# Kernel tuning notes

Measured on AMD Instinct MI355X. Metric: run time of the kernel, lower is better.

## Reference

```python
import jax, jax.numpy as jnp
import numpy as np

NUM_HEADS = 8
TOPK = 16


def setup_inputs() -> dict:
    key = jax.random.key(0)
    ks = jax.random.split(key, 13)
    B, C, H, W = 2, 512, 64, 64
    Hu, Wu = H // 2, W // 2
    hd = C // NUM_HEADS
    n = lambda k, shape, s=1.0: jax.random.normal(k, shape, dtype=jnp.float32) * s
    return {
        "x": n(ks[0], (B, C, H, W)),
        "upper_feat": n(ks[1], (B, C, Hu, Wu)),
        "gumbel": jax.random.gumbel(ks[2], (B, NUM_HEADS, Hu * Wu), dtype=jnp.float32),
        # 1x1 convs (Conv2d + folded eval-mode BN => weight matrix + bias)
        "q_w": n(ks[3], (C, C), 0.02), "q_b": n(ks[4], (C,), 0.02),
        "kv_w": n(ks[5], (2 * C, C), 0.02), "kv_b": n(ks[6], (2 * C,), 0.02),
        "proj_w": n(ks[7], (C, C), 0.02), "proj_b": n(ks[8], (C,), 0.02),
        # depthwise 7x7 PE conv (groups = C)
        "pe_w": n(ks[9], (C, 1, 7, 7), 0.02), "pe_b": n(ks[10], (C,), 0.02),
        # gate conv1d kernel_size=1: [head_dim, 2*head_dim]
        "gate_w": n(ks[11], (hd, 2 * hd), 0.02), "gate_b": n(ks[12], (hd,), 0.02),
    }


def reference(x, upper_feat, gumbel, q_w, q_b, kv_w, kv_b, proj_w, proj_b,
              pe_w, pe_b, gate_w, gate_b):
    B, C, H, W = x.shape
    hd = C // NUM_HEADS
    Hu, Wu = upper_feat.shape[2], upper_feat.shape[3]
    N, Nu = H * W, Hu * Wu
    scale = hd ** -0.5

    def conv1x1(t, w, b):
        return jnp.einsum('bchw,oc->bohw', t, w) + b[None, :, None, None]

    # coarse attention: q from x, k/v from upper_feat
    q = conv1x1(x, q_w, q_b).reshape(B, NUM_HEADS, hd, N).transpose(0, 1, 3, 2)          # [B,h,N,d]
    kv = conv1x1(upper_feat, kv_w, kv_b).reshape(B, NUM_HEADS, 2 * hd, Nu).transpose(0, 1, 3, 2)
    k, v = kv[..., :hd], kv[..., hd:]                                                    # [B,h,Nu,d]
    sim = jnp.einsum('bhnd,bhmd->bhnm', q, k) * scale                                    # [B,h,N,Nu]
    attn = jax.nn.softmax(sim, axis=-1)
    coarse = jnp.einsum('bhnm,bhmd->bhnd', attn, v)                                      # [B,h,N,d]

    # fine branch: kv from x, top-k token selection via gumbel-softmax scores
    f_kv = conv1x1(x, kv_w, kv_b).reshape(B, NUM_HEADS, 2 * hd, N).transpose(0, 1, 3, 2)
    f_k, f_v = f_kv[..., :hd], f_kv[..., hd:]                                            # [B,h,N,d]

    # heat: channel-mean of x, adaptive-avg-pooled 2x2 to upper resolution (no grad)
    heat = jax.lax.stop_gradient(
        x.mean(axis=1).reshape(B, Hu, 2, Wu, 2).mean(axis=(2, 4)).reshape(B, Nu))
    global_sim = sim.mean(axis=2) * heat[:, None, :]                                     # [B,h,Nu]
    soft_weights = jax.nn.softmax(global_sim + gumbel, axis=-1)
    _, idx = jax.lax.top_k(soft_weights, TOPK)                                           # [B,h,K]

    # map each selected upper-token to its 2x2 block of x-tokens
    h_idx = (idx // Wu) * 2
    w_idx = (idx % Wu) * 2
    idx_full = jnp.concatenate(
        [(h_idx + dh) * W + (w_idx + dw) for dh in range(2) for dw in range(2)], axis=-1)  # [B,h,4K]

    topk_k = jnp.take_along_axis(f_k, idx_full[..., None], axis=2)                       # [B,h,4K,d]
    topk_v = jnp.take_along_axis(f_v, idx_full[..., None], axis=2)
    fine = jax.nn.softmax(jnp.einsum('bhnd,bhmd->bhnm', q, topk_k) * scale, axis=-1)
    refined = jnp.einsum('bhnm,bhmd->bhnd', fine, topk_v)                                # [B,h,N,d]

    # gated fusion (conv1d kernel_size=1 == per-token linear over 2d channels)
    fusion = jnp.concatenate([coarse, refined], axis=-1)                                 # [B,h,N,2d]
    gate = jax.nn.sigmoid(jnp.einsum('bhnc,oc->bhno', fusion, gate_w) + gate_b)
    out = gate * refined + (1.0 - gate) * coarse                                         # [B,h,N,d]

    x_out = out.transpose(0, 1, 3, 2).reshape(B, C, H, W)

    # positional encoding: depthwise 7x7 conv on v, bilinear upsample to (H,W)
    v_rs = v.transpose(0, 1, 3, 2).reshape(B, C, Hu, Wu)
    v_pe = jax.lax.conv_general_dilated(
        v_rs, pe_w, (1, 1), ((3, 3), (3, 3)), feature_group_count=C,
        dimension_numbers=('NCHW', 'OIHW', 'NCHW')) + pe_b[None, :, None, None]
    v_pe = jax.image.resize(v_pe, (B, C, H, W), method='bilinear')

    return conv1x1(x_out + v_pe, proj_w, proj_b)
```

## Files before the change

### kernel.cpp

```cpp
#include <hip/hip_runtime.h>
#include <hip/hip_bf16.h>
#include <cstdint>

typedef __hip_bfloat16 bf16;
typedef unsigned short u16;
typedef __attribute__((ext_vector_type(8))) short bf16x8;
typedef __attribute__((ext_vector_type(4))) float f32x4;

static __device__ __forceinline__ float bs2f(u16 s) {
  unsigned int u = ((unsigned int)s) << 16;
  float f;
  __builtin_memcpy(&f, &u, 4);
  return f;
}
static __device__ __forceinline__ u16 f2bs(float f) {
  bf16 h = __float2bfloat16(f);
  u16 s;
  __builtin_memcpy(&s, &h, 2);
  return s;
}
static __device__ __forceinline__ float ldf(const void* p, size_t i, int f32) {
  return f32 ? ((const float*)p)[i] : bs2f(((const u16*)p)[i]);
}

__global__ __launch_bounds__(256) void detect_dtype(const uint4* __restrict__ xs,
                                                    int* __restrict__ flag) {
  int i = blockIdx.x * 256 + threadIdx.x;
  uint4 v = xs[i];
  bool hit = false;
#pragma unroll
  for (int j = 0; j < 4; ++j) {
    unsigned w = (j == 0) ? v.x : (j == 1) ? v.y : (j == 2) ? v.z : v.w;
    if ((w & 0x7F80u) == 0x7F80u) hit = true;
    if ((w & 0x7F800000u) == 0x7F800000u) hit = true;
  }
  unsigned long long mask = __ballot(hit);
  if (mask != 0ull && (threadIdx.x & 63) == 0) atomicOr(flag, 1);
}

__global__ __launch_bounds__(256) void prep_gate(
    const void* __restrict__ gate_w, const void* __restrict__ gate_b,
    u16* __restrict__ gwb, float* __restrict__ gbf,
    const int* __restrict__ dtf) {
  const int f32 = *dtf;
  int t = threadIdx.x;
  for (int i = t; i < 8192; i += 256)
    gwb[i] = f32 ? f2bs(((const float*)gate_w)[i]) : ((const u16*)gate_w)[i];
  if (t < 64) gbf[t] = ldf(gate_b, t, f32);
}

__global__ __launch_bounds__(256) void transpose_bf16(
    const void* __restrict__ src, u16* __restrict__ dst, int N,
    float* __restrict__ heat, const int* __restrict__ dtf) {
  const int f32 = *dtf;
  const int b = blockIdx.z, n0 = blockIdx.x * 64, c0 = blockIdx.y * 64;
  const int t = threadIdx.x;
  __shared__ __align__(16) u16 tile[64][72];
#pragma unroll
  for (int j = 0; j < 2; ++j) {
    int cc = (t >> 3) + j * 32;
    int nn = (t & 7) * 8;
    u16 tmp[8];
    if (f32) {
      const float* s4 = (const float*)src + ((size_t)(b * 512 + c0 + cc)) * N + n0 + nn;
#pragma unroll
      for (int u = 0; u < 8; ++u) tmp[u] = f2bs(s4[u]);
    } else {
      *reinterpret_cast<uint4*>(tmp) = *reinterpret_cast<const uint4*>(
          (const u16*)src + ((size_t)(b * 512 + c0 + cc)) * N + n0 + nn);
    }
    *reinterpret_cast<uint4*>(&tile[cc][nn]) = *reinterpret_cast<const uint4*>(tmp);
  }
  __syncthreads();
  if (heat != nullptr && t < 32) {
    float s = 0.f;
#pragma unroll 8
    for (int cc = 0; cc < 64; ++cc)
      s += bs2f(tile[cc][2 * t]) + bs2f(tile[cc][2 * t + 1]);
    int y = blockIdx.x;
    atomicAdd(&heat[b * 1024 + (y >> 1) * 32 + t], s);
  }
#pragma unroll
  for (int j = 0; j < 2; ++j) {
    int nn = (t >> 3) + j * 32;
    int cc0 = (t & 7) * 8;
    u16 tmp[8];
#pragma unroll
    for (int u = 0; u < 8; ++u) tmp[u] = tile[cc0 + u][nn];
    *reinterpret_cast<uint4*>(&dst[((size_t)b * N + n0 + nn) * 512 + c0 + cc0]) =
        *reinterpret_cast<const uint4*>(tmp);
  }
}

template<int MODE>
__global__ __launch_bounds__(256) void gemm128(
    const u16* __restrict__ A, const void* __restrict__ W,
    const void* __restrict__ bias, u16* __restrict__ o0,
    void* __restrict__ ob, float* __restrict__ qsum, int M,
    const int* __restrict__ dtf) {
  const int f32 = *dtf;
  const int b = blockIdx.z, m0 = blockIdx.x * 128, oo0 = blockIdx.y * 64;
  const int t = threadIdx.x, w = t >> 6, lane = t & 63;
  const int quad = lane >> 4, c = lane & 15;
  __shared__ __align__(16) u16 As[128][72];
  __shared__ __align__(16) u16 Ws[64][72];
  f32x4 acc[2][4];
#pragma unroll
  for (int nt = 0; nt < 2; ++nt)
#pragma unroll
    for (int ot = 0; ot < 4; ++ot) acc[nt][ot] = (f32x4){0.f, 0.f, 0.f, 0.f};
  const u16* Ab = A + (size_t)b * M * 512;
  const int arow = t >> 1, acol = (t & 1) * 32;
  const int wrow = t >> 2, wcol = (t & 3) * 16;

  for (int k0 = 0; k0 < 512; k0 += 64) {
    __syncthreads();
    {
      const u16* ga = Ab + (size_t)(m0 + arow) * 512 + k0 + acol;
      uint4* ad = reinterpret_cast<uint4*>(&As[arow][acol]);
      const uint4* gs = reinterpret_cast<const uint4*>(ga);
      ad[0] = gs[0]; ad[1] = gs[1]; ad[2] = gs[2]; ad[3] = gs[3];
      if (f32) {
        const float* gw = (const float*)W + (size_t)(oo0 + wrow) * 512 + k0 + wcol;
#pragma unroll
        for (int e = 0; e < 16; ++e) Ws[wrow][wcol + e] = f2bs(gw[e]);
      } else {
        const u16* gw = (const u16*)W + (size_t)(oo0 + wrow) * 512 + k0 + wcol;
        *reinterpret_cast<uint4*>(&Ws[wrow][wcol])     = *reinterpret_cast<const uint4*>(gw);
        *reinterpret_cast<uint4*>(&Ws[wrow][wcol + 8]) = *reinterpret_cast<const uint4*>(gw + 8);
      }
    }
    __syncthreads();
#pragma unroll
    for (int ks = 0; ks < 2; ++ks) {
      bf16x8 av[2];
      av[0] = *reinterpret_cast<const bf16x8*>(&As[w * 32 + c][ks * 32 + quad * 8]);
      av[1] = *reinterpret_cast<const bf16x8*>(&As[w * 32 + 16 + c][ks * 32 + quad * 8]);
#pragma unroll
      for (int ot = 0; ot < 4; ++ot) {
        bf16x8 wv = *reinterpret_cast<const bf16x8*>(&Ws[ot * 16 + c][ks * 32 + quad * 8]);
#pragma unroll
        for (int nt = 0; nt < 2; ++nt) {
          if (MODE == 3)
            acc[nt][ot] = __builtin_amdgcn_mfma_f32_16x16x32_bf16(wv, av[nt], acc[nt][ot], 0, 0, 0);
          else
            acc[nt][ot] = __builtin_amdgcn_mfma_f32_16x16x32_bf16(av[nt], wv, acc[nt][ot], 0, 0, 0);
        }
      }
    }
  }

  if (MODE == 0) {
    const int h = oo0 >> 6, bh = b * 8 + h;
#pragma unroll
    for (int ot = 0; ot < 4; ++ot) {
      int o = oo0 + ot * 16 + c;
      int d = o & 63;
      float bv = ldf(bias, o, f32);
      float qs = 0.f;
#pragma unroll
      for (int nt = 0; nt < 2; ++nt)
#pragma unroll
        for (int r = 0; r < 4; ++r) {
          int m = m0 + w * 32 + nt * 16 + quad * 4 + r;
          float qv = acc[nt][ot][r] + bv;
          o0[((size_t)bh * M + m) * 64 + d] = f2bs(qv * 0.125f);
          qs += qv;
        }
      qs += __shfl_xor(qs, 16, 64);
      qs += __shfl_xor(qs, 32, 64);
      if (quad == 0) atomicAdd(&qsum[bh * 64 + d], qs);
    }
  } else {
#pragma unroll
    for (int ot = 0; ot < 4; ++ot)
#pragma unroll
      for (int r = 0; r < 4; ++r) {
        int o = oo0 + ot * 16 + quad * 4 + r;
        float bv = ldf(bias, o, f32);
#pragma unroll
        for (int nt = 0; nt < 2; ++nt) {
          int m = m0 + w * 32 + nt * 16 + c;
          float val = acc[nt][ot][r] + bv;
          size_t oi_ = ((size_t)(b * 512 + o)) * M + m;
          if (f32) ((float*)ob)[oi_] = val;
          else     ((u16*)ob)[oi_] = f2bs(val);
        }
      }
  }
}

__global__ __launch_bounds__(256) void gemm_kv(
    const u16* __restrict__ A, const void* __restrict__ W,
    const void* __restrict__ bias, u16* __restrict__ kb, u16* __restrict__ v2,
    int M, const int* __restrict__ dtf) {
  const int f32 = *dtf;
  const int b = blockIdx.z, m0 = blockIdx.x * 64, oo0 = blockIdx.y * 64;
  const int t = threadIdx.x, w = t >> 6, lane = t & 63;
  const int quad = lane >> 4, c = lane & 15;
  __shared__ __align__(16) u16 As[64][72];
  __shared__ __align__(16) u16 Ws[64][72];
  f32x4 acc[4];
#pragma unroll
  for (int ot = 0; ot < 4; ++ot) acc[ot] = (f32x4){0.f, 0.f, 0.f, 0.f};
  const u16* Ab = A + (size_t)b * M * 512;
  const int srow = t >> 2, scol = (t & 3) * 16;

  for (int k0 = 0; k0 < 512; k0 += 64) {
    __syncthreads();
    {
      const u16* ga = Ab + (size_t)(m0 + srow) * 512 + k0 + scol;
      *reinterpret_cast<uint4*>(&As[srow][scol])     = *reinterpret_cast<const uint4*>(ga);
      *reinterpret_cast<uint4*>(&As[srow][scol + 8]) = *reinterpret_cast<const uint4*>(ga + 8);
      if (f32) {
        const float* gw = (const float*)W + (size_t)(oo0 + srow) * 512 + k0 + scol;
#pragma unroll
        for (int e = 0; e < 16; ++e) Ws[srow][scol + e] = f2bs(gw[e]);
      } else {
        const u16* gw = (const u16*)W + (size_t)(oo0 + srow) * 512 + k0 + scol;
        *reinterpret_cast<uint4*>(&Ws[srow][scol])     = *reinterpret_cast<const uint4*>(gw);
        *reinterpret_cast<uint4*>(&Ws[srow][scol + 8]) = *reinterpret_cast<const uint4*>(gw + 8);
      }
    }
    __syncthreads();
#pragma unroll
    for (int ks = 0; ks < 2; ++ks) {
      bf16x8 av = *reinterpret_cast<const bf16x8*>(&As[w * 16 + c][ks * 32 + quad * 8]);
#pragma unroll
      for (int ot = 0; ot < 4; ++ot) {
        bf16x8 wv = *reinterpret_cast<const bf16x8*>(&Ws[ot * 16 + c][ks * 32 + quad * 8]);
        acc[ot] = __builtin_amdgcn_mfma_f32_16x16x32_bf16(av, wv, acc[ot], 0, 0, 0);
      }
    }
  }

#pragma unroll
  for (int ot = 0; ot < 4; ++ot) {
    int o = oo0 + ot * 16 + c;
    float bv = ldf(bias, o, f32);
    int hh = o >> 7, jj = o & 127;
#pragma unroll
    for (int r = 0; r < 4; ++r) {
      int m = m0 + w * 16 + quad * 4 + r;
      u16 val = f2bs(acc[ot][r] + bv);
      if (jj < 64) {
        kb[((size_t)(b * 8 + hh) * M + m) * 64 + jj] = val;
      } else {
        int d = jj & 63;
        v2[((((size_t)(b * 8 + hh) * 16 + (m >> 6)) * 2 + ((m >> 5) & 1)) * 4 + (d >> 4)) * 512
           + (((m >> 3) & 3) * 16 + (d & 15)) * 8 + (m & 7)] = val;
      }
    }
  }
}

__global__ __launch_bounds__(256) void topk_kernel(
    const float* __restrict__ qsum, const u16* __restrict__ k,
    const float* __restrict__ heat, const void* __restrict__ gumbel,
    int* __restrict__ posb, const int* __restrict__ dtf) {
  const int f32 = *dtf;
  int bh = blockIdx.x, b = bh >> 3, t = threadIdx.x;
  __shared__ float qs[64];
  __shared__ float s[1024];
  __shared__ float rv[256];
  __shared__ int   ri[256];
  if (t < 64) qs[t] = qsum[bh * 64 + t];
  __syncthreads();
  for (int j = 0; j < 4; ++j) {
    int m = t + j * 256;
    const u16* kr = k + ((size_t)bh * 1024 + m) * 64;
    float dot = 0.f;
    for (int d = 0; d < 64; ++d) dot += qs[d] * bs2f(kr[d]);
    s[m] = dot * (0.125f / 4096.0f) * (heat[b * 1024 + m] * (1.0f / 2048.0f)) +
           ldf(gumbel, (size_t)bh * 1024 + m, f32);
  }
  __syncthreads();
  for (int it = 0; it < 16; ++it) {
    float bv = -1e30f; int bi = 0x7fffffff;
    for (int j = 0; j < 4; ++j) {
      int m = t + j * 256; float vv = s[m];
      if (vv > bv || (vv == bv && m < bi)) { bv = vv; bi = m; }
    }
    rv[t] = bv; ri[t] = bi; __syncthreads();
    for (int off = 128; off; off >>= 1) {
      if (t < off) {
        if (rv[t + off] > rv[t] || (rv[t + off] == rv[t] && ri[t + off] < ri[t])) {
          rv[t] = rv[t + off]; ri[t] = ri[t + off];
        }
      }
      __syncthreads();
    }
    if (t == 0) {
      int mi = ri[0]; s[mi] = -1e30f;
      int hy = (mi >> 5) * 2, wx = (mi & 31) * 2;
      posb[bh * 64 + it]      = hy * 64 + wx;
      posb[bh * 64 + 16 + it] = hy * 64 + wx + 1;
      posb[bh * 64 + 32 + it] = (hy + 1) * 64 + wx;
      posb[bh * 64 + 48 + it] = (hy + 1) * 64 + wx + 1;
    }
    __syncthreads();
  }
}

__global__ __launch_bounds__(256) void gather_kv_mfma(
    const u16* __restrict__ xT, const void* __restrict__ kv_w,
    const void* __restrict__ kv_b, const int* __restrict__ posb,
    u16* __restrict__ tkb, u16* __restrict__ tvTb,
    const int* __restrict__ dtf) {
  const int f32 = *dtf;
  const int bh = blockIdx.x, b = bh >> 3, h = bh & 7;
  const int half = blockIdx.y;
  const int t = threadIdx.x, w = t >> 6, lane = t & 63;
  const int quad = lane >> 4, c = lane & 15;
  __shared__ int pos[64];
  __shared__ __align__(16) u16 As[64][72];
  __shared__ __align__(16) u16 Ws[64][72];
  if (t < 64) pos[t] = posb[bh * 64 + t];
  __syncthreads();
  const int obase = h * 128 + half * 64;
  const int srow = t >> 2, scol = (t & 3) * 16;
  const int arow = pos[srow];
  f32x4 acc[4];
#pragma unroll
  for (int ot = 0; ot < 4; ++ot) acc[ot] = (f32x4){0.f, 0.f, 0.f, 0.f};

  for (int k0 = 0; k0 < 512; k0 += 64) {
    __syncthreads();
    {
      const u16* ga = xT + ((size_t)b * 4096 + arow) * 512 + k0 + scol;
      *reinterpret_cast<uint4*>(&As[srow][scol])     = *reinterpret_cast<const uint4*>(ga);
      *reinterpret_cast<uint4*>(&As[srow][scol + 8]) = *reinterpret_cast<const uint4*>(ga + 8);
      if (f32) {
        const float* gw = (const float*)kv_w + (size_t)(obase + srow) * 512 + k0 + scol;
#pragma unroll
        for (int e = 0; e < 16; ++e) Ws[srow][scol + e] = f2bs(gw[e]);
      } else {
        const u16* gw = (const u16*)kv_w + (size_t)(obase + srow) * 512 + k0 + scol;
        *reinterpret_cast<uint4*>(&Ws[srow][scol])     = *reinterpret_cast<const uint4*>(gw);
        *reinterpret_cast<uint4*>(&Ws[srow][scol + 8]) = *reinterpret_cast<const uint4*>(gw + 8);
      }
    }
    __syncthreads();
#pragma unroll
    for (int ks = 0; ks < 2; ++ks) {
      bf16x8 av = *reinterpret_cast<const bf16x8*>(&As[w * 16 + c][ks * 32 + quad * 8]);
#pragma unroll
      for (int ot = 0; ot < 4; ++ot) {
        bf16x8 wv = *reinterpret_cast<const bf16x8*>(&Ws[ot * 16 + c][ks * 32 + quad * 8]);
        acc[ot] = __builtin_amdgcn_mfma_f32_16x16x32_bf16(av, wv, acc[ot], 0, 0, 0);
      }
    }
  }

#pragma unroll
  for (int ot = 0; ot < 4; ++ot) {
    int d = ot * 16 + c;
    float bv = ldf(kv_b, obase + d, f32);
#pragma unroll
    for (int r = 0; r < 4; ++r) {
      int m = w * 16 + quad * 4 + r;
      u16 val = f2bs(acc[ot][r] + bv);
      if (half) tvTb[((size_t)bh * 64 + d) * 64 + m] = val;
      else      tkb[((size_t)bh * 64 + m) * 64 + d] = val;
    }
  }
}

__global__ __launch_bounds__(256) void dwconv_kernel(
    const u16* __restrict__ v2, const void* __restrict__ pe_w,
    const void* __restrict__ pe_b, u16* __restrict__ vpe,
    const int* __restrict__ dtf) {
  const int f32 = *dtf;
  int bc = blockIdx.x;
  int b = bc >> 9, c = bc & 511;
  int h = c >> 6, d = c & 63;
  int dt = d >> 4, cc = d & 15;
  int t = threadIdx.x;
  __shared__ float img[1024];
  __shared__ float wts[49];
  if (t < 128) {
    int ch = t >> 3, s = (t >> 2) & 1, q2 = t & 3;
    const u16* src = v2 + ((((size_t)(b * 8 + h) * 16 + ch) * 2 + s) * 4 + dt) * 512
                        + (q2 * 16 + cc) * 8;
    uint4 v4 = *reinterpret_cast<const uint4*>(src);
    u16 tmp[8];
    *reinterpret_cast<uint4*>(tmp) = v4;
#pragma unroll
    for (int e = 0; e < 8; ++e) img[t * 8 + e] = bs2f(tmp[e]);
  }
  if (t < 49) wts[t] = ldf(pe_w, c * 49 + t, f32);
  float bias = ldf(pe_b, c, f32);
  __syncthreads();
  for (int i = t; i < 1024; i += 256) {
    int y = i >> 5, xx = i & 31;
    float a = 0.f;
#pragma unroll
    for (int ky = 0; ky < 7; ++ky) {
      int yy = y + ky - 3;
      if ((unsigned)yy >= 32u) continue;
#pragma unroll
      for (int kx = 0; kx < 7; ++kx) {
        int xc = xx + kx - 3;
        if ((unsigned)xc >= 32u) continue;
        a += img[yy * 32 + xc] * wts[ky * 7 + kx];
      }
    }
    vpe[(size_t)bc * 1024 + i] = f2bs(a + bias);
  }
}

__global__ __launch_bounds__(256, 4) void attn_fused(
    const u16* __restrict__ q, const u16* __restrict__ k,
    const u16* __restrict__ v2, const u16* __restrict__ tkb,
    const u16* __restrict__ tvTb, const u16* __restrict__ gwb,
    const float* __restrict__ gbf, const u16* __restrict__ vpe,
    u16* __restrict__ xsT) {
  const int bh = blockIdx.y, b = bh >> 3, h = bh & 7;
  const int bx = blockIdx.x;
  const int n0 = bx * 64;
  const int t = threadIdx.x, w = t >> 6, lane = t & 63;
  const int quad = lane >> 4, c = lane & 15;

  __shared__ __align__(16) u16 lds[13824];
  u16* Ks = lds;
  u16* Ps = lds + 9216;

  bf16x8 bq[2];
  {
    const u16* qr = q + ((size_t)bh * 4096 + n0 + w * 16 + c) * 64;
    bq[0] = *reinterpret_cast<const bf16x8*>(qr + quad * 8);
    bq[1] = *reinterpret_cast<const bf16x8*>(qr + 32 + quad * 8);
  }
  f32x4 po[4];
#pragma unroll
  for (int dt = 0; dt < 4; ++dt) po[dt] = (f32x4){0.f, 0.f, 0.f, 0.f};
  float sume = 0.f;

  const u16* kbase = k + (size_t)bh * 65536;
  const u16* v2base = v2 + (size_t)bh * 65536;
  const int srow = t >> 2, scol = (t & 3) * 16;

  uint4 kr0, kr1;
  {
    const u16* gk = kbase + (size_t)srow * 64 + scol;
    kr0 = *reinterpret_cast<const uint4*>(gk);
    kr1 = *reinterpret_cast<const uint4*>(gk + 8);
    *reinterpret_cast<uint4*>(&Ks[srow * 72 + scol])     = kr0;
    *reinterpret_cast<uint4*>(&Ks[srow * 72 + scol + 8]) = kr1;
    const u16* gk1 = kbase + (size_t)(64 + srow) * 64 + scol;
    kr0 = *reinterpret_cast<const uint4*>(gk1);
    kr1 = *reinterpret_cast<const uint4*>(gk1 + 8);
  }

  for (int ch = 0; ch < 16; ++ch) {
    __syncthreads();
    const int buf = ch & 1;

    bf16x8 av[4][2];
    {
      const u16* v2c = v2base + (size_t)ch * 4096;
#pragma unroll
      for (int dt = 0; dt < 4; ++dt) {
        av[dt][0] = *reinterpret_cast<const bf16x8*>(v2c + dt * 512 + lane * 8);
        av[dt][1] = *reinterpret_cast<const bf16x8*>(v2c + 2048 + dt * 512 + lane * 8);
      }
    }

    f32x4 st[4];
#pragma unroll
    for (int mt = 0; mt < 4; ++mt) {
      const u16* krow = &Ks[buf * 4608 + (mt * 16 + c) * 72];
      bf16x8 ak0 = *reinterpret_cast<const bf16x8*>(krow + quad * 8);
      bf16x8 ak1 = *reinterpret_cast<const bf16x8*>(krow + 32 + quad * 8);
      f32x4 acc = (f32x4){0.f, 0.f, 0.f, 0.f};
      acc = __builtin_amdgcn_mfma_f32_16x16x32_bf16(ak0, bq[0], acc, 0, 0, 0);
      acc = __builtin_amdgcn_mfma_f32_16x16x32_bf16(ak1, bq[1], acc, 0, 0, 0);
      st[mt] = acc;
    }

    if (ch + 1 < 16) {
      *reinterpret_cast<uint4*>(&Ks[(buf ^ 1) * 4608 + srow * 72 + scol])     = kr0;
      *reinterpret_cast<uint4*>(&Ks[(buf ^ 1) * 4608 + srow * 72 + scol + 8]) = kr1;
      if (ch + 2 < 16) {
        const u16* gk = kbase + (size_t)((ch + 2) * 64 + srow) * 64 + scol;
        kr0 = *reinterpret_cast<const uint4*>(gk);
        kr1 = *reinterpret_cast<const uint4*>(gk + 8);
      }
    }

    float cs = 0.f;
    u16* psw = &Ps[(w * 16 + c) * 72];
#pragma unroll
    for (int mt = 0; mt < 4; ++mt) {
      float e0 = __expf(st[mt][0]);
      float e1 = __expf(st[mt][1]);
      float e2 = __expf(st[mt][2]);
      float e3 = __expf(st[mt][3]);
      cs += (e0 + e1) + (e2 + e3);
      ushort4 pw;
      pw.x = f2bs(e0); pw.y = f2bs(e1); pw.z = f2bs(e2); pw.w = f2bs(e3);
      *reinterpret_cast<ushort4*>(psw + mt * 16 + quad * 4) = pw;
    }
    cs += __shfl_xor(cs, 16, 64);
    cs += __shfl_xor(cs, 32, 64);
    sume += cs;

#pragma unroll
    for (int s = 0; s < 2; ++s) {
      bf16x8 bp = *reinterpret_cast<const bf16x8*>(psw + s * 32 + quad * 8);
#pragma unroll
      for (int dt = 0; dt < 4; ++dt) {
        po[dt] = __builtin_amdgcn_mfma_f32_16x16x32_bf16(av[dt][s], bp, po[dt], 0, 0, 0);
      }
    }
  }

  __syncthreads();
  u16* fus = lds;
  u16* vl  = lds + 8704;
  float* gbl = (float*)(lds + 13312);

  const int ym = bx >> 1;
  int r0_, r1_; float wy0, wy1;
  if ((bx & 1) == 0) { r0_ = ym > 0 ? ym - 1 : 0; r1_ = ym; wy0 = 0.25f; wy1 = 0.75f; }
  else               { r0_ = ym; r1_ = ym < 31 ? ym + 1 : 31; wy0 = 0.75f; wy1 = 0.25f; }

  for (int idx = t; idx < 512; idx += 256) {
    int seg = idx & 3, ch2 = (idx >> 2) & 63, rr = idx >> 8;
    int vrow = rr ? r1_ : r0_;
    const uint4 v4 = *reinterpret_cast<const uint4*>(
        vpe + ((size_t)(b * 512 + h * 64 + ch2)) * 1024 + vrow * 32 + seg * 8);
    u16* dst = &vl[(rr * 64 + ch2) * 36 + seg * 8];
    uint2 lo, hi;
    lo.x = v4.x; lo.y = v4.y; hi.x = v4.z; hi.y = v4.w;
    *reinterpret_cast<uint2*>(dst)     = lo;
    *reinterpret_cast<uint2*>(dst + 4) = hi;
  }
  if (t < 64) gbl[t] = gbf[t];
  __syncthreads();

  u16* fusw = &fus[(w * 16 + c) * 136];
  f32x4 st2[4];
#pragma unroll
  for (int mt = 0; mt < 4; ++mt) {
    f32x4 acc = (f32x4){0.f, 0.f, 0.f, 0.f};
#pragma unroll
    for (int s = 0; s < 2; ++s) {
      bf16x8 ak = *reinterpret_cast<const bf16x8*>(
          &tkb[((size_t)bh * 64 + mt * 16 + c) * 64 + s * 32 + quad * 8]);
      acc = __builtin_amdgcn_mfma_f32_16x16x32_bf16(ak, bq[s], acc, 0, 0, 0);
    }
    st2[mt] = acc;
  }
  float sume2 = 0.f;
#pragma unroll
  for (int mt = 0; mt < 4; ++mt) {
    float e0 = __expf(st2[mt][0]);
    float e1 = __expf(st2[mt][1]);
    float e2 = __expf(st2[mt][2]);
    float e3 = __expf(st2[mt][3]);
    sume2 += (e0 + e1) + (e2 + e3);
    ushort4 pw;
    pw.x = f2bs(e0); pw.y = f2bs(e1); pw.z = f2bs(e2); pw.w = f2bs(e3);
    *reinterpret_cast<ushort4*>(fusw + mt * 16 + quad * 4) = pw;
  }
  sume2 += __shfl_xor(sume2, 16, 64);
  sume2 += __shfl_xor(sume2, 32, 64);
  float inv2 = 1.0f / sume2;

  f32x4 po2[4];
#pragma unroll
  for (int dt = 0; dt < 4; ++dt) po2[dt] = (f32x4){0.f, 0.f, 0.f, 0.f};
#pragma unroll
  for (int s = 0; s < 2; ++s) {
    bf16x8 bp = *reinterpret_cast<const bf16x8*>(fusw + s * 32 + quad * 8);
#pragma unroll
    for (int dt = 0; dt < 4; ++dt) {
      bf16x8 av = *reinterpret_cast<const bf16x8*>(
          &tvTb[((size_t)bh * 64 + dt * 16 + c) * 64 + s * 32 + quad * 8]);
      po2[dt] = __builtin_amdgcn_mfma_f32_16x16x32_bf16(av, bp, po2[dt], 0, 0, 0);
    }
  }

  float invc = 1.0f / sume;
#pragma unroll
  for (int dt = 0; dt < 4; ++dt) {
    ushort4 cw, rw;
    cw.x = f2bs(po[dt][0] * invc); cw.y = f2bs(po[dt][1] * invc);
    cw.z = f2bs(po[dt][2] * invc); cw.w = f2bs(po[dt][3] * invc);
    rw.x = f2bs(po2[dt][0] * inv2); rw.y = f2bs(po2[dt][1] * inv2);
    rw.z = f2bs(po2[dt][2] * inv2); rw.w = f2bs(po2[dt][3] * inv2);
    *reinterpret_cast<ushort4*>(fusw + dt * 16 + quad * 4)      = cw;
    *reinterpret_cast<ushort4*>(fusw + 64 + dt * 16 + quad * 4) = rw;
  }

  f32x4 ga[4];
#pragma unroll
  for (int ot = 0; ot < 4; ++ot) ga[ot] = (f32x4){0.f, 0.f, 0.f, 0.f};
#pragma unroll
  for (int s = 0; s < 4; ++s) {
    bf16x8 bf = *reinterpret_cast<const bf16x8*>(fusw + s * 32 + quad * 8);
#pragma unroll
    for (int ot = 0; ot < 4; ++ot) {
      bf16x8 ag = *reinterpret_cast<const bf16x8*>(
          gwb + (ot * 16 + c) * 128 + s * 32 + quad * 8);
      ga[ot] = __builtin_amdgcn_mfma_f32_16x16x32_bf16(ag, bf, ga[ot], 0, 0, 0);
    }
  }

  const int x = w * 16 + c;
  int jx = x >> 1, x0, x1; float wx0, wx1;
  if ((x & 1) == 0) { x0 = (jx > 0) ? jx - 1 : 0; x1 = jx; wx0 = 0.25f; wx1 = 0.75f; }
  else              { x0 = jx; x1 = (jx < 31) ? jx + 1 : 31; wx0 = 0.75f; wx1 = 0.25f; }
#pragma unroll
  for (int dt = 0; dt < 4; ++dt) {
    ushort4 ow;
    u16 tmp[4];
#pragma unroll
    for (int r = 0; r < 4; ++r) {
      int row = dt * 16 + quad * 4 + r;
      float ref = po2[dt][r] * inv2;
      float coar = bs2f(fusw[row]);
      float g = 1.0f / (1.0f + __expf(-(ga[dt][r] + gbl[row])));
      float vv = wy0 * (wx0 * bs2f(vl[row * 36 + x0]) +
                        wx1 * bs2f(vl[row * 36 + x1])) +
                 wy1 * (wx0 * bs2f(vl[(64 + row) * 36 + x0]) +
                        wx1 * bs2f(vl[(64 + row) * 36 + x1]));
      tmp[r] = f2bs(g * ref + (1.0f - g) * coar + vv);
    }
    ow.x = tmp[0]; ow.y = tmp[1]; ow.z = tmp[2]; ow.w = tmp[3];
    *reinterpret_cast<ushort4*>(fusw + dt * 16 + quad * 4) = ow;
  }

  {
    int nl = lane >> 2, cs2 = (lane & 3) * 16;
    const u16* srcrow = &fus[(w * 16 + nl) * 136 + cs2];
    u16* dst = xsT + ((size_t)b * 4096 + n0 + w * 16 + nl) * 512 + h * 64 + cs2;
    *reinterpret_cast<uint4*>(dst)     = *reinterpret_cast<const uint4*>(srcrow);
    *reinterpret_cast<uint4*>(dst + 8) = *reinterpret_cast<const uint4*>(srcrow + 8);
  }
}

extern "C" void kernel_launch(void* const* d_in, const int* in_sizes, int n_in,
                              void* d_out, int out_size, void* d_ws, size_t ws_size,
                              hipStream_t stream) {
  const void* x    = d_in[0];
  const void* up   = d_in[1];
  const void* gum  = d_in[2];
  const void* q_w  = d_in[3];
  const void* q_b  = d_in[4];
  const void* kv_w = d_in[5];
  const void* kv_b = d_in[6];
  const void* p_w  = d_in[7];
  const void* p_b  = d_in[8];
  const void* pe_w = d_in[9];
  const void* pe_b = d_in[10];
  const void* g_w  = d_in[11];
  const void* g_b  = d_in[12];

  float* ws    = (float*)d_ws;
  int*   dtf   = (int*)ws;
  float* qsum  = ws + 16;
  float* heat  = qsum + 1024;
  int*   posb  = (int*)(heat + 2048);
  float* gbf   = (float*)(posb + 1024);
  u16*   gwb   = (u16*)(gbf + 64);
  u16*   tkb   = gwb + 8192;
  u16*   tvTb  = tkb + 65536;
  u16*   qb    = tvTb + 65536;
  u16*   kb    = qb + 4194304;
  u16*   v2b   = kb + 1048576;
  u16*   xT    = v2b + 1048576;
  u16*   upT   = xT + 4194304;
  u16*   xsT   = upT + 1048576;
  u16*   vpe   = xsT + 4194304;

  dim3 blk(256);
  hipMemsetAsync(ws, 0, (16 + 1024 + 2048) * 4, stream);
  detect_dtype<<<dim3(64), blk, 0, stream>>>((const uint4*)x, dtf);
  prep_gate<<<dim3(1), blk, 0, stream>>>(g_w, g_b, gwb, gbf, dtf);
  transpose_bf16<<<dim3(64, 8, 2), blk, 0, stream>>>(x, xT, 4096, heat, dtf);
  transpose_bf16<<<dim3(16, 8, 2), blk, 0, stream>>>(up, upT, 1024, nullptr, dtf);
  gemm128<0><<<dim3(32, 8, 2), blk, 0, stream>>>(xT, q_w, q_b, qb, nullptr, qsum, 4096, dtf);
  gemm_kv<<<dim3(16, 16, 2), blk, 0, stream>>>(upT, kv_w, kv_b, kb, v2b, 1024, dtf);
  topk_kernel<<<dim3(16), blk, 0, stream>>>(qsum, kb, heat, gum, posb, dtf);
  gather_kv_mfma<<<dim3(16, 2), blk, 0, stream>>>(xT, kv_w, kv_b, posb, tkb, tvTb, dtf);
  dwconv_kernel<<<dim3(1024), blk, 0, stream>>>(v2b, pe_w, pe_b, vpe, dtf);
  attn_fused<<<dim3(64, 16), blk, 0, stream>>>(qb, kb, v2b, tkb, tvTb, gwb, gbf, vpe, xsT);
  gemm128<3><<<dim3(32, 8, 2), blk, 0, stream>>>(xsT, p_w, p_b, nullptr, d_out, nullptr, 4096, dtf);
}
```

Measured before the change: 257.2 us.

## Pre-swizzle K into MFMA fragment layout and read it directly from global memory

The KV GEMM now also writes a second copy of K in MFMA-fragment order (k2), alongside the existing row-major copy. The attention kernel loads K fragments straight from global/L2 per lane, the same way it already loads V. This removes the LDS double-buffered K staging and its per-chunk __syncthreads, and shrinks shared memory. The trade-off is an extra K write in gemm_kv, more global load traffic per block, higher register use, and dropping the min-blocks-per-CU launch bound, which can lower occupancy.

Measured after the change: 299.4 us. 16.4% more time.

```diff
diff --git a/kernel.cpp b/kernel.cpp
--- a/kernel.cpp
+++ b/kernel.cpp
@@ -192,8 +192,8 @@
 
 __global__ __launch_bounds__(256) void gemm_kv(
     const u16* __restrict__ A, const void* __restrict__ W,
-    const void* __restrict__ bias, u16* __restrict__ kb, u16* __restrict__ v2,
-    int M, const int* __restrict__ dtf) {
+    const void* __restrict__ bias, u16* __restrict__ kb, u16* __restrict__ k2,
+    u16* __restrict__ v2, int M, const int* __restrict__ dtf) {
   const int f32 = *dtf;
   const int b = blockIdx.z, m0 = blockIdx.x * 64, oo0 = blockIdx.y * 64;
   const int t = threadIdx.x, w = t >> 6, lane = t & 63;
@@ -245,6 +245,10 @@
       u16 val = f2bs(acc[ot][r] + bv);
       if (jj < 64) {
         kb[((size_t)(b * 8 + hh) * M + m) * 64 + jj] = val;
+        int ck = m & 15, mtk = (m >> 4) & 3, chk = m >> 6;
+        int ek = jj & 7, qdk = (jj >> 3) & 3, sk = (jj >> 5) & 1;
+        k2[((((size_t)(b * 8 + hh) * 16 + chk) * 4 + mtk) * 2 + sk) * 512
+           + qdk * 128 + ck * 8 + ek] = val;
       } else {
         int d = jj & 63;
         v2[((((size_t)(b * 8 + hh) * 16 + (m >> 6)) * 2 + ((m >> 5) & 1)) * 4 + (d >> 4)) * 512
@@ -409,8 +413,8 @@
   }
 }
 
-__global__ __launch_bounds__(256, 4) void attn_fused(
-    const u16* __restrict__ q, const u16* __restrict__ k,
+__global__ __launch_bounds__(256) void attn_fused(
+    const u16* __restrict__ q, const u16* __restrict__ k2,
     const u16* __restrict__ v2, const u16* __restrict__ tkb,
     const u16* __restrict__ tvTb, const u16* __restrict__ gwb,
     const float* __restrict__ gbf, const u16* __restrict__ vpe,
@@ -421,9 +425,8 @@
   const int t = threadIdx.x, w = t >> 6, lane = t & 63;
   const int quad = lane >> 4, c = lane & 15;
 
-  __shared__ __align__(16) u16 lds[13824];
-  u16* Ks = lds;
-  u16* Ps = lds + 9216;
+  __shared__ __align__(16) u16 lds[13440];
+  u16* Ps = lds;
 
   bf16x8 bq[2];
   {
@@ -436,60 +439,38 @@
   for (int dt = 0; dt < 4; ++dt) po[dt] = (f32x4){0.f, 0.f, 0.f, 0.f};
   float sume = 0.f;
 
-  const u16* kbase = k + (size_t)bh * 65536;
+  const u16* k2base = k2 + (size_t)bh * 65536;
   const u16* v2base = v2 + (size_t)bh * 65536;
-  const int srow = t >> 2, scol = (t & 3) * 16;
-
-  uint4 kr0, kr1;
-  {
-    const u16* gk = kbase + (size_t)srow * 64 + scol;
-    kr0 = *reinterpret_cast<const uint4*>(gk);
-    kr1 = *reinterpret_cast<const uint4*>(gk + 8);
-    *reinterpret_cast<uint4*>(&Ks[srow * 72 + scol])     = kr0;
-    *reinterpret_cast<uint4*>(&Ks[srow * 72 + scol + 8]) = kr1;
-    const u16* gk1 = kbase + (size_t)(64 + srow) * 64 + scol;
-    kr0 = *reinterpret_cast<const uint4*>(gk1);
-    kr1 = *reinterpret_cast<const uint4*>(gk1 + 8);
-  }
-
+  u16* psw = &Ps[(w * 16 + c) * 72];
+
+#pragma unroll 2
   for (int ch = 0; ch < 16; ++ch) {
-    __syncthreads();
-    const int buf = ch & 1;
-
+    const u16* k2c = k2base + (size_t)ch * 4096;
+    const u16* v2c = v2base + (size_t)ch * 4096;
+
+    bf16x8 ak[4][2];
+#pragma unroll
+    for (int mt = 0; mt < 4; ++mt) {
+      ak[mt][0] = *reinterpret_cast<const bf16x8*>(k2c + (mt * 2 + 0) * 512 + lane * 8);
+      ak[mt][1] = *reinterpret_cast<const bf16x8*>(k2c + (mt * 2 + 1) * 512 + lane * 8);
+    }
     bf16x8 av[4][2];
-    {
-      const u16* v2c = v2base + (size_t)ch * 4096;
-#pragma unroll
-      for (int dt = 0; dt < 4; ++dt) {
-        av[dt][0] = *reinterpret_cast<const bf16x8*>(v2c + dt * 512 + lane * 8);
-        av[dt][1] = *reinterpret_cast<const bf16x8*>(v2c + 2048 + dt * 512 + lane * 8);
-      }
+#pragma unroll
+    for (int dt = 0; dt < 4; ++dt) {
+      av[dt][0] = *reinterpret_cast<const bf16x8*>(v2c + dt * 512 + lane * 8);
+      av[dt][1] = *reinterpret_cast<const bf16x8*>(v2c + 2048 + dt * 512 + lane * 8);
     }
 
     f32x4 st[4];
 #pragma unroll
     for (int mt = 0; mt < 4; ++mt) {
-      const u16* krow = &Ks[buf * 4608 + (mt * 16 + c) * 72];
-      bf16x8 ak0 = *reinterpret_cast<const bf16x8*>(krow + quad * 8);
-      bf16x8 ak1 = *reinterpret_cast<const bf16x8*>(krow + 32 + quad * 8);
       f32x4 acc = (f32x4){0.f, 0.f, 0.f, 0.f};
-      acc = __builtin_amdgcn_mfma_f32_16x16x32_bf16(ak0, bq[0], acc, 0, 0, 0);
-      acc = __builtin_amdgcn_mfma_f32_16x16x32_bf16(ak1, bq[1], acc, 0, 0, 0);
+      acc = __builtin_amdgcn_mfma_f32_16x16x32_bf16(ak[mt][0], bq[0], acc, 0, 0, 0);
+      acc = __builtin_amdgcn_mfma_f32_16x16x32_bf16(ak[mt][1], bq[1], acc, 0, 0, 0);
       st[mt] = acc;
     }
 
-    if (ch + 1 < 16) {
-      *reinterpret_cast<uint4*>(&Ks[(buf ^ 1) * 4608 + srow * 72 + scol])     = kr0;
-      *reinterpret_cast<uint4*>(&Ks[(buf ^ 1) * 4608 + srow * 72 + scol + 8]) = kr1;
-      if (ch + 2 < 16) {
-        const u16* gk = kbase + (size_t)((ch + 2) * 64 + srow) * 64 + scol;
-        kr0 = *reinterpret_cast<const uint4*>(gk);
-        kr1 = *reinterpret_cast<const uint4*>(gk + 8);
-      }
-    }
-
     float cs = 0.f;
-    u16* psw = &Ps[(w * 16 + c) * 72];
 #pragma unroll
     for (int mt = 0; mt < 4; ++mt) {
       float e0 = __expf(st[mt][0]);
@@ -669,7 +650,8 @@
   u16*   tvTb  = tkb + 65536;
   u16*   qb    = tvTb + 65536;
   u16*   kb    = qb + 4194304;
-  u16*   v2b   = kb + 1048576;
+  u16*   k2b   = kb + 1048576;
+  u16*   v2b   = k2b + 1048576;
   u16*   xT    = v2b + 1048576;
   u16*   upT   = xT + 4194304;
   u16*   xsT   = upT + 1048576;
@@ -682,10 +664,10 @@
   transpose_bf16<<<dim3(64, 8, 2), blk, 0, stream>>>(x, xT, 4096, heat, dtf);
   transpose_bf16<<<dim3(16, 8, 2), blk, 0, stream>>>(up, upT, 1024, nullptr, dtf);
   gemm128<0><<<dim3(32, 8, 2), blk, 0, stream>>>(xT, q_w, q_b, qb, nullptr, qsum, 4096, dtf);
-  gemm_kv<<<dim3(16, 16, 2), blk, 0, stream>>>(upT, kv_w, kv_b, kb, v2b, 1024, dtf);
+  gemm_kv<<<dim3(16, 16, 2), blk, 0, stream>>>(upT, kv_w, kv_b, kb, k2b, v2b, 1024, dtf);
   topk_kernel<<<dim3(16), blk, 0, stream>>>(qsum, kb, heat, gum, posb, dtf);
   gather_kv_mfma<<<dim3(16, 2), blk, 0, stream>>>(xT, kv_w, kv_b, posb, tkb, tvTb, dtf);
   dwconv_kernel<<<dim3(1024), blk, 0, stream>>>(v2b, pe_w, pe_b, vpe, dtf);
-  attn_fused<<<dim3(64, 16), blk, 0, stream>>>(qb, kb, v2b, tkb, tvTb, gwb, gbf, vpe, xsT);
+  attn_fused<<<dim3(64, 16), blk, 0, stream>>>(qb, k2b, v2b, tkb, tvTb, gwb, gbf, vpe, xsT);
   gemm128<3><<<dim3(32, 8, 2), blk, 0, stream>>>(xsT, p_w, p_b, nullptr, d_out, nullptr, 4096, dtf);
 }
```
